# Kernel optimization log

Measured on AMD Instinct MI355X. Metric: run time of the kernel, lower is better.

The kernel has to match this reference:

```python
import jax, jax.numpy as jnp
import numpy as np
import math

INPUT_SZ = 1024
HIDDEN_SZ = 1024
BATCH = 64
SEQ = 512


def setup_inputs() -> dict:
    key = jax.random.key(0)
    ks = jax.random.split(key, 9)
    stdv = 1.0 / math.sqrt(HIDDEN_SZ)
    def u(k, shape):
        return jax.random.uniform(k, shape, jnp.float32, -stdv, stdv)
    W_shape = (INPUT_SZ + HIDDEN_SZ, HIDDEN_SZ)
    return {
        "x": jax.random.normal(ks[0], (BATCH, SEQ, INPUT_SZ), jnp.float32),
        "Wf": u(ks[1], W_shape), "bf": u(ks[2], (HIDDEN_SZ,)),
        "Wi": u(ks[3], W_shape), "bi": u(ks[4], (HIDDEN_SZ,)),
        "Wc": u(ks[5], W_shape), "bc": u(ks[6], (HIDDEN_SZ,)),
        "Wo": u(ks[7], W_shape), "bo": u(ks[8], (HIDDEN_SZ,)),
    }


def _lstm_cummax(x, Wf, bf, Wi, bi, Wc, bc, Wo, bo):
    B, S, _ = x.shape
    H = Wf.shape[1]
    # Concatenate the 4 gate matmuls into one GEMM (same math as 4 separate ones).
    W = jnp.concatenate([Wf, Wi, Wc, Wo], axis=1)  # (H+I, 4H)
    b = jnp.concatenate([bf, bi, bc, bo])          # (4H,)

    h0 = jnp.zeros((B, H), x.dtype)
    C0 = jnp.zeros((B, H), x.dtype)
    hmax0 = jnp.full((B, H), -jnp.inf, x.dtype)

    def step(carry, xt):
        h_in, Ct, hmax = carry
        hx = jnp.concatenate([h_in, xt], axis=1)   # (B, H+I), h first (matches torch cat((ht, xt)))
        g = hx @ W + b                             # (B, 4H)
        ft = jax.nn.sigmoid(g[:, :H])
        it = jax.nn.sigmoid(g[:, H:2 * H])
        cc = jnp.tanh(g[:, 2 * H:3 * H])
        ot = jax.nn.sigmoid(g[:, 3 * H:])
        Ct = ft * Ct + it * cc
        h = ot * jnp.tanh(Ct)                      # raw per-step hidden, stored in output seq
        hmax = jnp.maximum(hmax, h)                # running max over all steps so far
        # next-step input hidden is the running max (at t=0, max == h0 anyway)
        return (hmax, Ct, hmax), h

    (h_fin, C_fin, _), hs = jax.lax.scan(step, (h0, C0, hmax0), jnp.swapaxes(x, 0, 1))
    hidden_seq = jnp.swapaxes(hs, 0, 1)            # (B, S, H), raw per-step hiddens
    return hidden_seq, (h_fin, C_fin)


def reference(x, Wf, bf, Wi, bi, Wc, bc, Wo, bo):
    return _lstm_cummax(x, Wf, bf, Wi, bi, Wc, bc, Wo, bo)
```

## Files before the change

kernel.cpp:

```cpp
#include <hip/hip_runtime.h>
#include <hip/hip_bf16.h>
#include <math.h>
#include <stddef.h>

#define S_LEN 512
#define NBATCH 64
#define HID 1024
#define IN_SZ 1024
#define KTOT 2048
#define NB 128
#define NCOLS 32
#define JPB 8

using short8  = __attribute__((ext_vector_type(8))) short;
using floatx4 = __attribute__((ext_vector_type(4))) float;

static const size_t WPACK_OFF = 0;
static const size_t XBF_OFF   = 16777216;
static const size_t HBUF_OFF  = XBF_OFF + 67108864;
static const size_t FLAGS_OFF = HBUF_OFF + 67239936;

__device__ __forceinline__ unsigned short f2b(float f) {
  __hip_bfloat16 h = __float2bfloat16(f);
  return *reinterpret_cast<unsigned short*>(&h);
}
__device__ __forceinline__ float sigm(float z) {
  z = fminf(fmaxf(z, -30.f), 30.f);
  return 1.f / (1.f + __expf(-z));
}
__device__ __forceinline__ float tanh_(float z) {
  z = fminf(fmaxf(z, -15.f), 15.f);
  float e = __expf(2.f * z);
  return (e - 1.f) / (e + 1.f);
}

__global__ void prep_w(const float* __restrict__ Wf, const float* __restrict__ Wi,
                       const float* __restrict__ Wc, const float* __restrict__ Wo,
                       __hip_bfloat16* __restrict__ wpack) {
  __shared__ float tile[64][65];
  const int g = blockIdx.z;
  const float* W = (g == 0) ? Wf : (g == 1) ? Wi : (g == 2) ? Wc : Wo;
  const int k0 = blockIdx.x * 64, j0 = blockIdx.y * 64;
  const int tx = threadIdx.x, ty = threadIdx.y;
  for (int kk = 0; kk < 64; kk += 4)
    tile[kk + ty][tx] = W[(size_t)(k0 + kk + ty) * HID + j0 + tx];
  __syncthreads();
  for (int jj = 0; jj < 64; jj += 4) {
    int j = j0 + jj + ty;
    size_t out = ((size_t)((j >> 3) * NCOLS + g * 8 + (j & 7))) * KTOT + k0 + tx;
    wpack[out] = __float2bfloat16(tile[tx][jj + ty]);
  }
}

__global__ void prep_x(const float* __restrict__ x, unsigned short* __restrict__ xbf,
                       int* __restrict__ flags) {
  size_t i = ((size_t)blockIdx.x * blockDim.x + threadIdx.x) * 4;
  float4 v = *(const float4*)(x + i);
  ushort4 u;
  u.x = f2b(v.x); u.y = f2b(v.y); u.z = f2b(v.z); u.w = f2b(v.w);
  *(ushort4*)(xbf + i) = u;
  if (blockIdx.x == 0 && threadIdx.x < NB) flags[threadIdx.x] = 0;
}

__launch_bounds__(256, 1)
__global__ void lstm_rec(const unsigned short* __restrict__ xbf,
                         const unsigned short* __restrict__ wpack,
                         const float* __restrict__ bfv, const float* __restrict__ biv,
                         const float* __restrict__ bcv, const float* __restrict__ bov,
                         unsigned short* __restrict__ hbuf,
                         int* __restrict__ flags,
                         float* __restrict__ out) {
  __shared__ float part[4][64][36];
  const int tid  = threadIdx.x;
  const int w    = tid >> 6;
  const int lane = tid & 63;
  const int l15  = lane & 15;
  const int lq   = lane >> 4;
  const int p    = blockIdx.x;
  const int j0   = p * JPB;

  short8 Wreg[32];
  {
    const unsigned short* wp = wpack + (size_t)p * NCOLS * KTOT;
#pragma unroll
    for (int ks = 0; ks < 16; ++ks)
#pragma unroll
      for (int n = 0; n < 2; ++n) {
        int c = n * 16 + l15;
        int k = w * 512 + ks * 32 + lq * 8;
        Wreg[ks * 2 + n] = *(const short8*)(wp + (size_t)c * KTOT + k);
      }
  }
  float bias0, bias1;
  {
    int c = l15;
    bias0 = (c < 8) ? bfv[j0 + c] : biv[j0 + c - 8];
    bias1 = (c < 8) ? bcv[j0 + c] : bov[j0 + c - 8];
  }
  float Cst[4]  = {0.f, 0.f, 0.f, 0.f};
  float hmax[4] = {-__builtin_inff(), -__builtin_inff(), -__builtin_inff(), -__builtin_inff()};
  const int  jj    = l15 & 7;
  const bool act   = (l15 < 8);
  const int  bbase = w * 16 + lq * 4;
  const bool is_x  = (w >= 2);

  for (int t = 0; t < S_LEN; ++t) {
    floatx4 acc[4][2];
#pragma unroll
    for (int m = 0; m < 4; ++m) { acc[m][0] = (floatx4){0,0,0,0}; acc[m][1] = (floatx4){0,0,0,0}; }

    if (is_x) {
      const unsigned short* xa = xbf + (size_t)t * IN_SZ + (w - 2) * 512 + lq * 8;
#pragma unroll
      for (int ks = 0; ks < 16; ++ks) {
        short8 a[4];
#pragma unroll
        for (int m = 0; m < 4; ++m)
          a[m] = *(const short8*)(xa + (size_t)(m * 16 + l15) * ((size_t)S_LEN * IN_SZ) + ks * 32);
#pragma unroll
        for (int m = 0; m < 4; ++m) {
          acc[m][0] = __builtin_amdgcn_mfma_f32_16x16x32_bf16(a[m], Wreg[ks * 2 + 0], acc[m][0], 0, 0, 0);
          acc[m][1] = __builtin_amdgcn_mfma_f32_16x16x32_bf16(a[m], Wreg[ks * 2 + 1], acc[m][1], 0, 0, 0);
        }
      }
    } else if (t > 0) {
      {
        bool ready;
        do {
          int a = __hip_atomic_load(&flags[lane],      __ATOMIC_RELAXED, __HIP_MEMORY_SCOPE_AGENT);
          int b = __hip_atomic_load(&flags[lane + 64], __ATOMIC_RELAXED, __HIP_MEMORY_SCOPE_AGENT);
          ready = __all((a >= t) && (b >= t));
        } while (!ready);
        __atomic_signal_fence(__ATOMIC_ACQUIRE);
      }
      const unsigned short* ha = hbuf + (size_t)t * (NBATCH * HID) + w * 512 + lq * 8;
#pragma unroll
      for (int ks = 0; ks < 16; ++ks) {
        short8 a[4];
#pragma unroll
        for (int m = 0; m < 4; ++m)
          a[m] = *(const short8*)(ha + (size_t)(m * 16 + l15) * HID + ks * 32);
#pragma unroll
        for (int m = 0; m < 4; ++m) {
          acc[m][0] = __builtin_amdgcn_mfma_f32_16x16x32_bf16(a[m], Wreg[ks * 2 + 0], acc[m][0], 0, 0, 0);
          acc[m][1] = __builtin_amdgcn_mfma_f32_16x16x32_bf16(a[m], Wreg[ks * 2 + 1], acc[m][1], 0, 0, 0);
        }
      }
    }
#pragma unroll
    for (int m = 0; m < 4; ++m) {
      *(floatx4*)&part[w][lane][m * 8 + 0] = acc[m][0];
      *(floatx4*)&part[w][lane][m * 8 + 4] = acc[m][1];
    }
    __syncthreads();
    floatx4 r0 = {0, 0, 0, 0}, r1 = {0, 0, 0, 0};
#pragma unroll
    for (int sw = 0; sw < 4; ++sw) {
      r0 += *(const floatx4*)&part[sw][lane][w * 8 + 0];
      r1 += *(const floatx4*)&part[sw][lane][w * 8 + 4];
    }
#pragma unroll
    for (int r = 0; r < 4; ++r) {
      float g0  = r0[r] + bias0;
      float g1  = r1[r] + bias1;
      float g0o = __shfl_xor(g0, 8);
      float g1o = __shfl_xor(g1, 8);
      float fg = sigm(g0);
      float ig = sigm(g0o);
      float cg = tanh_(g1);
      float og = sigm(g1o);
      float C  = fg * Cst[r] + ig * cg;
      Cst[r] = C;
      float h = og * tanh_(C);
      int b = bbase + r;
      if (act)
        out[(size_t)b * ((size_t)S_LEN * HID) + (size_t)t * HID + j0 + jj] = h;
      float hm = fmaxf(hmax[r], h);
      hmax[r] = hm;
      unsigned int hb    = f2b(hm);
      unsigned int other = (unsigned int)__shfl_xor((int)hb, 1) & 0xffffu;
      if (act && ((jj & 1) == 0)) {
        unsigned int word = hb | (other << 16);
        unsigned int* dst = (unsigned int*)(hbuf + (size_t)(t + 1) * (NBATCH * HID) + (size_t)b * HID + j0 + jj);
        __hip_atomic_store(dst, word, __ATOMIC_RELAXED, __HIP_MEMORY_SCOPE_AGENT);
      }
    }
    __syncthreads();
    if (tid == 0)
      __hip_atomic_store(&flags[p], t + 1, __ATOMIC_RELAXED, __HIP_MEMORY_SCOPE_AGENT);
  }
  const size_t HSEQ = (size_t)NBATCH * S_LEN * HID;
#pragma unroll
  for (int r = 0; r < 4; ++r) {
    int b = bbase + r;
    if (act) {
      out[HSEQ + (size_t)b * HID + j0 + jj] = hmax[r];
      out[HSEQ + (size_t)NBATCH * HID + (size_t)b * HID + j0 + jj] = Cst[r];
    }
  }
}

extern "C" void kernel_launch(void* const* d_in, const int* in_sizes, int n_in,
                              void* d_out, int out_size, void* d_ws, size_t ws_size,
                              hipStream_t stream) {
  const float* x   = (const float*)d_in[0];
  const float* Wf  = (const float*)d_in[1];
  const float* bf_ = (const float*)d_in[2];
  const float* Wi  = (const float*)d_in[3];
  const float* bi_ = (const float*)d_in[4];
  const float* Wc  = (const float*)d_in[5];
  const float* bc_ = (const float*)d_in[6];
  const float* Wo  = (const float*)d_in[7];
  const float* bo_ = (const float*)d_in[8];
  char* ws = (char*)d_ws;
  __hip_bfloat16* wpack_bf = (__hip_bfloat16*)(ws + WPACK_OFF);
  unsigned short* xbf      = (unsigned short*)(ws + XBF_OFF);
  unsigned short* hbuf     = (unsigned short*)(ws + HBUF_OFF);
  int* flags               = (int*)(ws + FLAGS_OFF);
  float* outp              = (float*)d_out;

  hipLaunchKernelGGL(prep_w, dim3(KTOT / 64, HID / 64, 4), dim3(64, 4, 1), 0, stream,
                     Wf, Wi, Wc, Wo, wpack_bf);
  hipLaunchKernelGGL(prep_x, dim3(32768), dim3(256), 0, stream, x, xbf, flags);

  lstm_rec<<<dim3(NB), dim3(256), 0, stream>>>(
      xbf, (const unsigned short*)wpack_bf, bf_, bi_, bc_, bo_, hbuf, flags, outp);
}
```

Baseline: 6.870 ms.

## Stage hidden state in LDS, store it in a packed per-block layout, defer output writes

Each block now collects its bf16 hmax values and fp32 h outputs in shared memory. It then writes the recurrent state to hbuf as one contiguous 1KB chunk per block instead of scattered 4-byte stores across batch rows, and consumers read the A fragments with a matching layout. The flag poll uses one 64-bit load per lane instead of two 32-bit loads. The hidden-sequence output is written with vectorized nontemporal stores by the x-side waves after the flag is published. This takes global writes off the critical path, at the cost of an extra __syncthreads per step.

```diff
diff --git a/kernel.cpp b/kernel.cpp
--- a/kernel.cpp
+++ b/kernel.cpp
@@ -71,6 +71,8 @@
                          int* __restrict__ flags,
                          float* __restrict__ out) {
   __shared__ float part[4][64][36];
+  __shared__ unsigned short hsl[NBATCH * JPB];
+  __shared__ float          osl[NBATCH * JPB];
   const int tid  = threadIdx.x;
   const int w    = tid >> 6;
   const int lane = tid & 63;
@@ -127,19 +129,21 @@
       {
         bool ready;
         do {
-          int a = __hip_atomic_load(&flags[lane],      __ATOMIC_RELAXED, __HIP_MEMORY_SCOPE_AGENT);
-          int b = __hip_atomic_load(&flags[lane + 64], __ATOMIC_RELAXED, __HIP_MEMORY_SCOPE_AGENT);
+          long long ff = __hip_atomic_load((const long long*)flags + lane,
+                                           __ATOMIC_RELAXED, __HIP_MEMORY_SCOPE_AGENT);
+          int a = (int)ff, b = (int)(ff >> 32);
           ready = __all((a >= t) && (b >= t));
         } while (!ready);
         __atomic_signal_fence(__ATOMIC_ACQUIRE);
       }
-      const unsigned short* ha = hbuf + (size_t)t * (NBATCH * HID) + w * 512 + lq * 8;
+      const unsigned short* hab = hbuf + (size_t)t * (NBATCH * HID)
+                                 + (size_t)w * 32768 + (size_t)lq * 512 + (size_t)l15 * 8;
 #pragma unroll
       for (int ks = 0; ks < 16; ++ks) {
         short8 a[4];
 #pragma unroll
         for (int m = 0; m < 4; ++m)
-          a[m] = *(const short8*)(ha + (size_t)(m * 16 + l15) * HID + ks * 32);
+          a[m] = *(const short8*)(hab + ks * 2048 + m * 128);
 #pragma unroll
         for (int m = 0; m < 4; ++m) {
           acc[m][0] = __builtin_amdgcn_mfma_f32_16x16x32_bf16(a[m], Wreg[ks * 2 + 0], acc[m][0], 0, 0, 0);
@@ -172,30 +176,40 @@
       float C  = fg * Cst[r] + ig * cg;
       Cst[r] = C;
       float h = og * tanh_(C);
-      int b = bbase + r;
-      if (act)
-        out[(size_t)b * ((size_t)S_LEN * HID) + (size_t)t * HID + j0 + jj] = h;
       float hm = fmaxf(hmax[r], h);
       hmax[r] = hm;
-      unsigned int hb    = f2b(hm);
-      unsigned int other = (unsigned int)__shfl_xor((int)hb, 1) & 0xffffu;
-      if (act && ((jj & 1) == 0)) {
-        unsigned int word = hb | (other << 16);
-        unsigned int* dst = (unsigned int*)(hbuf + (size_t)(t + 1) * (NBATCH * HID) + (size_t)b * HID + j0 + jj);
-        __hip_atomic_store(dst, word, __ATOMIC_RELAXED, __HIP_MEMORY_SCOPE_AGENT);
-      }
+      if (act) {
+        int b = bbase + r;
+        osl[b * JPB + l15] = h;
+        hsl[b * JPB + l15] = f2b(hm);
+      }
+    }
+    __syncthreads();
+    {
+      unsigned word = *((const unsigned*)hsl + tid);
+      unsigned* dst = (unsigned*)(hbuf + (size_t)(t + 1) * (NBATCH * HID)
+                                  + (size_t)p * 512) + tid;
+      __hip_atomic_store(dst, word, __ATOMIC_RELAXED, __HIP_MEMORY_SCOPE_AGENT);
     }
     __syncthreads();
     if (tid == 0)
       __hip_atomic_store(&flags[p], t + 1, __ATOMIC_RELAXED, __HIP_MEMORY_SCOPE_AGENT);
+    if (is_x) {
+      int q    = tid - 128;
+      int b    = q >> 1;
+      int half = q & 1;
+      floatx4 v = *(const floatx4*)&osl[b * JPB + half * 4];
+      __builtin_nontemporal_store(
+          v, (floatx4*)&out[(size_t)b * ((size_t)S_LEN * HID) + (size_t)t * HID + j0 + half * 4]);
+    }
   }
   const size_t HSEQ = (size_t)NBATCH * S_LEN * HID;
 #pragma unroll
   for (int r = 0; r < 4; ++r) {
     int b = bbase + r;
     if (act) {
-      out[HSEQ + (size_t)b * HID + j0 + jj] = hmax[r];
-      out[HSEQ + (size_t)NBATCH * HID + (size_t)b * HID + j0 + jj] = Cst[r];
+      __builtin_nontemporal_store(hmax[r], &out[HSEQ + (size_t)b * HID + j0 + jj]);
+      __builtin_nontemporal_store(Cst[r],  &out[HSEQ + (size_t)NBATCH * HID + (size_t)b * HID + j0 + jj]);
     }
   }
 }
```

Measured after the change: 5.685 ms. -17.3%, faster.
